# Kernel tuning notes

Measured on AMD Instinct MI355X. Metric: run time of the kernel, lower is better.

Reference implementation:

```python
import jax, jax.numpy as jnp
import numpy as np

HID = 128          # args.hidden_dim
B = 8              # batch_size
N = 256            # num_nodes per graph (uniform)
L = 48             # num_colours / levels per graph (uniform, logk=False)
CELLS = B * N * L  # 98304 'cell' nodes
E = 250000         # edges per edge type
STEPS = 2          # args.msg_passing_steps


def setup_inputs() -> dict:
    key = jax.random.key(0)
    ks = jax.random.split(key, 20)
    s = 0.05
    d = {}
    d["q"] = jax.random.randint(ks[0], (CELLS,), 0, 3)
    d["edge_src"] = jax.random.randint(ks[1], (2, E), 0, CELLS)
    d["edge_dst"] = jax.random.randint(ks[2], (2, E), 0, CELLS)
    d["embed"] = jax.random.normal(ks[3], (3, HID), jnp.float32) * s
    # per-edge-type 4-layer MLP (stacked along axis 0: [intra, inter])
    d["msg_W0"] = jax.random.normal(ks[4], (2, HID, 2 * HID), jnp.float32) * s
    d["msg_b0"] = jnp.zeros((2, HID), jnp.float32)
    d["msg_W1"] = jax.random.normal(ks[5], (2, HID, HID), jnp.float32) * s
    d["msg_b1"] = jnp.zeros((2, HID), jnp.float32)
    d["msg_W2"] = jax.random.normal(ks[6], (2, HID, HID), jnp.float32) * s
    d["msg_b2"] = jnp.zeros((2, HID), jnp.float32)
    d["msg_W3"] = jax.random.normal(ks[7], (2, HID, HID), jnp.float32) * s
    d["msg_b3"] = jnp.zeros((2, HID), jnp.float32)
    # LSTMCell, bias=False: input = cat(x, m_intra, m_inter) -> 3*HID
    d["lstm_Wih"] = jax.random.normal(ks[8], (4 * HID, 3 * HID), jnp.float32) * s
    d["lstm_Whh"] = jax.random.normal(ks[9], (4 * HID, HID), jnp.float32) * s
    d["score_w"] = jax.random.normal(ks[10], (1, HID), jnp.float32) * s
    return d


def reference(q, edge_src, edge_dst, embed, msg_W0, msg_b0, msg_W1, msg_b1,
              msg_W2, msg_b2, msg_W3, msg_b3, lstm_Wih, lstm_Whh, score_w):
    x = embed[q]  # [CELLS, HID]

    def edge_msgs(h):
        msgs = []
        for et in range(2):  # structural loop over the 2 edge types
            src, dst = edge_src[et], edge_dst[et]
            m = jnp.concatenate([h[src], h[dst]], axis=-1)  # [E, 2H]
            m = jax.nn.relu(m @ msg_W0[et].T + msg_b0[et])
            m = jax.nn.relu(m @ msg_W1[et].T + msg_b1[et])
            m = jax.nn.relu(m @ msg_W2[et].T + msg_b2[et])
            m = m @ msg_W3[et].T + msg_b3[et]
            msgs.append(jax.ops.segment_sum(m, dst, num_segments=CELLS))
        return msgs

    def step(carry, _):
        h, rh, rc = carry
        m_intra, m_inter = edge_msgs(h)
        lstm_in = jnp.concatenate([x, m_intra, m_inter], axis=-1)  # [CELLS, 3H]
        gates = lstm_in @ lstm_Wih.T + rh @ lstm_Whh.T              # [CELLS, 4H]
        i, f, g, o = jnp.split(gates, 4, axis=-1)
        nc = jax.nn.sigmoid(f) * rc + jax.nn.sigmoid(i) * jnp.tanh(g)
        nh = jax.nn.sigmoid(o) * jnp.tanh(nc)
        return (nh, nh, nc), nh

    zeros = jnp.zeros_like(x)
    _, outs = jax.lax.scan(step, (x, zeros, zeros), None, length=STEPS)
    # outs: [STEPS, CELLS, HID]; uniform sizes make get_padded_tensor a reshape:
    # [STEPS, B, L, N, HID] -> score -> view(STEPS, B*N*L)
    logits = (outs @ score_w[0]).reshape(STEPS, B * L * N)
    return logits
```

## Files before the change

kernel.cpp:

```cpp
#include <hip/hip_runtime.h>

#define HID 128
#define CELLS 98304
#define NE 250000
#define NSTEPS 2
#define NWIN 3912

typedef __attribute__((ext_vector_type(8))) short short8;
typedef __attribute__((ext_vector_type(4))) float f32x4;
typedef __attribute__((ext_vector_type(4))) unsigned int u32x4;
typedef unsigned short u16;

__device__ __forceinline__ int permf(int s) { return ((s & 7) << 4) | (s >> 3); }
__device__ __forceinline__ int nat_of_pos(int p) {
  int l = p & 63, hf = p >> 6;
  int slot = ((l >> 2) << 3) + (hf << 2) + (l & 3);
  return ((slot & 7) << 4) | (slot >> 3);
}

__device__ __forceinline__ u16 f2bf(float f) {
  unsigned int u = __builtin_bit_cast(unsigned int, f);
  u += 0x7fffu + ((u >> 16) & 1u);
  return (u16)(u >> 16);
}
__device__ __forceinline__ float bf2f(u16 s) {
  unsigned int u = ((unsigned int)s) << 16;
  return __builtin_bit_cast(float, u);
}
__device__ __forceinline__ unsigned int cvtpk_bf16(float lo, float hi) {
  unsigned int r;
  asm("v_cvt_pk_bf16_f32 %0, %1, %2" : "=v"(r) : "v"(lo), "v"(hi));
  return r;
}
__device__ __forceinline__ float sigm(float x) { return 1.f / (1.f + __expf(-x)); }
__device__ __forceinline__ float tanha(float x) { return 1.f - 2.f / (__expf(2.f * x) + 1.f); }

__device__ __forceinline__ void gload_lds16(const u16* g, u16* l) {
  __builtin_amdgcn_global_load_lds(
      (const __attribute__((address_space(1))) unsigned int*)(const void*)g,
      (__attribute__((address_space(3))) unsigned int*)(void*)l, 16, 0, 0);
}

__device__ __forceinline__ void stage_w(const u16* __restrict__ ws, u16* wl, int w, int lane) {
  #pragma unroll
  for (int i = 0; i < 2; ++i)
    gload_lds16(ws + i * 4096 + w * 512 + lane * 8, wl + i * 4096 + w * 512);
}

__global__ void prep_kernel(
    const float* __restrict__ W0, const float* __restrict__ W1,
    const float* __restrict__ W2, const float* __restrict__ W3,
    const float* __restrict__ b0, const float* __restrict__ b1,
    const float* __restrict__ b2, const float* __restrict__ b3,
    const float* __restrict__ Wih, const float* __restrict__ Whh,
    const float* __restrict__ embed, const float* __restrict__ sw,
    u16* __restrict__ W0b, u16* __restrict__ W123b,
    u16* __restrict__ Wcb, float* __restrict__ bp,
    u16* __restrict__ embp, float* __restrict__ swp)
{
  int idx = blockIdx.x * 256 + threadIdx.x;
  if (idx < 65536) {
    int et = idx >> 15, t = (idx >> 13) & 3, n = (idx >> 6) & 127, s = idx & 63;
    int g = s >> 3, j = s & 7;
    int gn = g ^ (n & 7);
    W0b[idx] = f2bf(W0[(et * 128 + n) * 256 + t * 64 + gn * 8 + j]);
    return;
  }
  idx -= 65536;
  if (idx < 98304) {
    int which = idx >> 15, r = idx & 32767;
    int et = r >> 14, hh = (r >> 13) & 1, n = (r >> 6) & 127, s = r & 63;
    int g = s >> 3, j = s & 7;
    int gn = g ^ (n & 7);
    const float* W = which == 0 ? W1 : (which == 1 ? W2 : W3);
    W123b[which * 32768 + r] = f2bf(W[(et * 128 + n) * 128 + permf(hh * 64 + gn * 8 + j)]);
    return;
  }
  idx -= 98304;
  if (idx < 262144) {
    int s = idx & 511, n = idx >> 9;
    int blk = s >> 7, s7 = s & 127;
    int k7 = (blk == 1 || blk == 2) ? nat_of_pos(s7) : s7;
    float v = (blk < 3) ? Wih[n * 384 + blk * 128 + k7] : Whh[n * 128 + k7];
    Wcb[idx] = f2bf(v);
    return;
  }
  idx -= 262144;
  if (idx < 1024) {
    int l = idx >> 8, r = idx & 255;
    int et = r >> 7, s = r & 127;
    const float* b = l == 0 ? b0 : (l == 1 ? b1 : (l == 2 ? b2 : b3));
    bp[idx] = b[et * 128 + permf(s)];
    return;
  }
  idx -= 1024;
  if (idx < 384) {
    embp[idx] = f2bf(embed[idx]);
    return;
  }
  idx -= 384;
  if (idx < 128) swp[idx] = sw[idx];
}

__global__ void init_kernel(const int* __restrict__ q, const u16* __restrict__ embp,
                            u16* __restrict__ xb, u16* __restrict__ h)
{
  int idx = blockIdx.x * 256 + threadIdx.x;
  int c = idx >> 7, s = idx & 127;
  u16 v = embp[q[c] * 128 + s];
  xb[idx] = v;
  h[idx] = v;
}

__global__ void hist_kernel(const int* __restrict__ edst, int* __restrict__ counts)
{
  int idx = blockIdx.x * 256 + threadIdx.x;
  if (idx >= 2 * NE) return;
  int et = (idx >= NE) ? 1 : 0;
  atomicAdd(&counts[et * CELLS + edst[idx]], 1);
}

__global__ void scan1_kernel(const int* __restrict__ counts, int* __restrict__ S,
                             int* __restrict__ btot)
{
  __shared__ int sh[1024];
  const int t = threadIdx.x, b = blockIdx.x;
  const int i = b * 1024 + t;
  int v = counts[i];
  sh[t] = v;
  __syncthreads();
  int acc = v;
  for (int off = 1; off < 1024; off <<= 1) {
    int add = (t >= off) ? sh[t - off] : 0;
    __syncthreads();
    acc += add;
    sh[t] = acc;
    __syncthreads();
  }
  S[i] = acc - v;
  if (t == 1023) btot[b] = acc;
}

__global__ void scan2_kernel(const int* __restrict__ btot, int* __restrict__ boffs,
                             int* __restrict__ S)
{
  __shared__ int sh[256];
  const int t = threadIdx.x;
  int v = (t < 192) ? btot[t] : 0;
  sh[t] = v;
  __syncthreads();
  int acc = v;
  for (int off = 1; off < 256; off <<= 1) {
    int add = (t >= off) ? sh[t - off] : 0;
    __syncthreads();
    acc += add;
    sh[t] = acc;
    __syncthreads();
  }
  if (t < 192) boffs[t] = acc - v;
  if (t == 0) S[2 * CELLS] = 2 * NE;
}

__global__ void scan3_kernel(int* __restrict__ S, const int* __restrict__ boffs)
{
  const int i = blockIdx.x * 1024 + threadIdx.x;
  S[i] += boffs[blockIdx.x];
}

__global__ void scatter_kernel(const int* __restrict__ esrc, const int* __restrict__ edst,
                               const int* __restrict__ S, int* __restrict__ fill,
                               int* __restrict__ ssrc, int* __restrict__ sdst)
{
  int idx = blockIdx.x * 256 + threadIdx.x;
  if (idx >= 2 * NE) return;
  int et = (idx >= NE) ? 1 : 0;
  int d = edst[idx];
  int pos = atomicAdd(&fill[et * CELLS + d], 1);
  int slot = S[et * CELLS + d] - et * NE + pos;
  sdst[et * NE + slot] = d;
  ssrc[et * NE + slot] = esrc[idx];
}

__device__ __forceinline__ void bias_relu_store(f32x4 (&acc)[4][8], const float* __restrict__ bl,
                                                u16* __restrict__ ab, int q, int c)
{
  float bias[8];
  #pragma unroll
  for (int j = 0; j < 8; ++j) bias[j] = bl[c * 8 + j];
  #pragma unroll
  for (int mt = 0; mt < 4; ++mt) {
    #pragma unroll
    for (int r = 0; r < 4; ++r) {
      const int rowl = mt * 16 + 4 * q + r;
      u32x4 t;
      #pragma unroll
      for (int p = 0; p < 4; ++p) {
        float v0 = acc[mt][2 * p][r] + bias[2 * p];
        float v1 = acc[mt][2 * p + 1][r] + bias[2 * p + 1];
        v0 = v0 > 0.f ? v0 : 0.f;
        v1 = v1 > 0.f ? v1 : 0.f;
        t[p] = cvtpk_bf16(v0, v1);
      }
      *(u32x4*)(ab + rowl * 128 + ((c ^ (rowl & 15)) << 3)) = t;
    }
  }
}

__launch_bounds__(512, 2)
__global__ void msg_kernel(
    const u16* __restrict__ h,
    const int* __restrict__ ssrc, const int* __restrict__ sdst,
    const int* __restrict__ S,
    const u16* __restrict__ W0b, const u16* __restrict__ W123b,
    const float* __restrict__ bp,
    u16* __restrict__ m0, u16* __restrict__ m1,
    int* __restrict__ side_dst, float* __restrict__ side_part)
{
  __shared__ u16 abuf[8][64 * 128];
  __shared__ u16 wbuf[2][128 * 64];
  const int et = blockIdx.y;
  const int tid = threadIdx.x;
  const int w = tid >> 6, lane = tid & 63, q = lane >> 4, c = lane & 15;
  const int ebase = blockIdx.x * 512 + w * 64;
  const int win = blockIdx.x * 8 + w;
  const int* __restrict__ src = ssrc + et * NE;
  const int* __restrict__ dst = sdst + et * NE;
  u16* __restrict__ msgs = (et == 0) ? m0 : m1;
  u16* ab = abuf[w];

  int eS = ebase + lane;
  if (eS >= NE) eS = NE - 1;
  const int srow = src[eS];

  int rowD[4];
  #pragma unroll
  for (int mt = 0; mt < 4; ++mt) {
    int e = ebase + mt * 16 + c;
    if (e >= NE) e = NE - 1;
    rowD[mt] = dst[e];
  }

  #pragma unroll
  for (int i = 0; i < 16; ++i) {
    const int r = i * 4 + (lane >> 4);
    const int grow = __shfl(srow, r);
    const int cg = lane & 15;
    gload_lds16(h + (size_t)grow * 128 + ((cg ^ (r & 15)) << 3), ab + i * 512);
  }
  stage_w(W0b + (et * 4 + 2) * 8192, wbuf[0], w, lane);

  const int eL = ebase + lane;
  const int dval = (eL < NE) ? dst[eL] : -1;
  int rpS = 0, rpE = 0;
  if (dval >= 0) {
    rpS = S[et * CELLS + dval] - et * NE;
    rpE = S[et * CELLS + dval + 1] - et * NE;
  }
  const int dlagged = __shfl_up(dval, 1);
  const bool headp = (lane == 0) | (dval != dlagged);
  const unsigned long long tails = (__ballot(headp) >> 1) | (1ull << 63);
  const unsigned long long intmask = __ballot(dval >= 0 && rpS >= ebase && rpE <= ebase + 64);

  const f32x4 zf = {0.f, 0.f, 0.f, 0.f};
  f32x4 acc[4][8];
  #pragma unroll
  for (int mt = 0; mt < 4; ++mt)
    #pragma unroll
    for (int nt = 0; nt < 8; ++nt) acc[mt][nt] = zf;

  asm volatile("s_waitcnt vmcnt(0)" ::: "memory");
  __syncthreads();

  #pragma unroll 1
  for (int i = 0; i < 10; ++i) {
    if (i < 9) {
      const int j = i + 1;
      const u16* wsrc;
      if (j < 4) {
        const int t = (j < 2) ? (j + 2) : (j - 2);
        wsrc = W0b + (et * 4 + t) * 8192;
      } else {
        const int li = j - 4;
        wsrc = W123b + (li >> 1) * 32768 + et * 16384 + (li & 1) * 8192;
      }
      stage_w(wsrc, wbuf[j & 1], w, lane);
    }
    if (i >= 4 && !(i & 1)) {
      bias_relu_store(acc, bp + ((i - 4) >> 1) * 256 + et * 128, ab, q, c);
      #pragma unroll
      for (int mt = 0; mt < 4; ++mt)
        #pragma unroll
        for (int nt = 0; nt < 8; ++nt) acc[mt][nt] = zf;
    }
    const u16* wb = wbuf[i & 1];
    #pragma unroll
    for (int ks = 0; ks < 2; ++ks) {
      short8 a[4], b[8];
      if (i < 2) {
        const int kqh = i * 64 + ks * 32 + q * 8;
        #pragma unroll
        for (int mt = 0; mt < 4; ++mt)
          a[mt] = *(const short8*)(h + (size_t)rowD[mt] * HID + kqh);
      } else {
        const int blk = (i & 1) * 8 + ks * 4 + q;
        #pragma unroll
        for (int mt = 0; mt < 4; ++mt) {
          const int row = mt * 16 + c;
          a[mt] = *(const short8*)(ab + row * 128 + ((blk ^ c) << 3));
        }
      }
      #pragma unroll
      for (int nt = 0; nt < 8; ++nt)
        b[nt] = *(const short8*)(wb + (nt * 16 + c) * 64 + (((ks * 4 + q) ^ (c & 7)) << 3));
      #pragma unroll
      for (int mt = 0; mt < 4; ++mt)
        #pragma unroll
        for (int nt = 0; nt < 8; ++nt)
          acc[mt][nt] = __builtin_amdgcn_mfma_f32_16x16x32_bf16(a[mt], b[nt], acc[mt][nt], 0, 0, 0);
    }
    asm volatile("s_waitcnt vmcnt(0)" ::: "memory");
    __syncthreads();
  }

  float bias[8];
  #pragma unroll
  for (int j = 0; j < 8; ++j) bias[j] = bp[3 * 256 + et * 128 + c * 8 + j];

  float* fab = (float*)ab;
  #pragma unroll
  for (int half = 0; half < 2; ++half) {
    #pragma unroll
    for (int mt = 0; mt < 4; ++mt) {
      #pragma unroll
      for (int r = 0; r < 4; ++r) {
        const int row = mt * 16 + 4 * q + r;
        f32x4 t;
        #pragma unroll
        for (int nti = 0; nti < 4; ++nti)
          t[nti] = acc[mt][half * 4 + nti][r] + bias[half * 4 + nti];
        *(f32x4*)(fab + row * 64 + c * 4) = t;
      }
    }
    float run = 0.f;
    int jstart = 0;
    #pragma unroll 1
    for (int jb = 0; jb < 64; jb += 8) {
      #pragma unroll
      for (int u = 0; u < 8; ++u) {
        const int j = jb + u;
        run += fab[j * 64 + lane];
        if ((tails >> j) & 1) {
          const int d = __builtin_amdgcn_readlane(dval, j);
          if (d >= 0) {
            if ((intmask >> j) & 1) {
              msgs[(size_t)d * HID + half * 64 + lane] = f2bf(run);
            } else {
              const int slot = (jstart == 0) ? 0 : 1;
              const size_t sb = ((size_t)et * NWIN + win) * 2 + slot;
              side_part[sb * 128 + half * 64 + lane] = run;
              if (lane == 0 && half == 0) side_dst[sb] = d;
            }
          }
          run = 0.f;
          jstart = j + 1;
        }
      }
    }
  }
}

__global__ void fixup_kernel(const int* __restrict__ S,
                             const int* __restrict__ side_dst,
                             const float* __restrict__ side_part,
                             u16* __restrict__ m0, u16* __restrict__ m1)
{
  const int b = blockIdx.x;
  const int et = b / NWIN, win = b - et * NWIN;
  const int t = threadIdx.x;
  u16* __restrict__ m = et ? m1 : m0;
  #pragma unroll
  for (int s = 0; s < 2; ++s) {
    const int d = side_dst[b * 2 + s];
    if (d < 0) continue;
    const int r0 = S[et * CELLS + d] - et * NE;
    if ((r0 >> 6) != win) continue;
    const int w1 = (S[et * CELLS + d + 1] - et * NE - 1) >> 6;
    float sum = 0.f;
    for (int wi = win; wi <= w1; ++wi) {
      const int base = (et * NWIN + wi) * 2;
      if (side_dst[base + 0] == d) sum += side_part[(size_t)(base + 0) * 128 + t];
      if (side_dst[base + 1] == d) sum += side_part[(size_t)(base + 1) * 128 + t];
    }
    m[(size_t)d * HID + t] = f2bf(sum);
  }
}

__launch_bounds__(512, 4)
__global__ void lstm_kernel(
    const int step,
    const u16* __restrict__ xb, const u16* __restrict__ mm0, const u16* __restrict__ mm1,
    u16* __restrict__ h, u16* __restrict__ rc,
    const u16* __restrict__ Wcb, const float* __restrict__ swp,
    float* __restrict__ out)
{
  __shared__ u16 at[64 * 512];
  const int tid = threadIdx.x;
  const int cb = blockIdx.x * 64;

  for (int base = tid * 8; base < 64 * 512; base += 4096) {
    const int cl = base >> 9, s = base & 511;
    const int cell = cb + cl;
    short8 t;
    if (s < 128) {
      t = *(const short8*)(xb + cell * 128 + s);
    } else if (s < 384) {
      const u16* mp = (s < 256 ? mm0 : mm1) + cell * 128 + (s & 127);
      t = *(const short8*)(mp);
    } else if (step == 0) {
      #pragma unroll
      for (int j = 0; j < 8; ++j) t[j] = 0;
    } else {
      t = *(const short8*)(h + cell * 128 + (s & 127));
    }
    const int blk = s >> 3;
    const int blks = (blk & 48) | ((blk ^ cl) & 15);
    *(short8*)(at + cl * 512 + blks * 8) = t;
  }
  __syncthreads();

  const int w = tid >> 6, lane = tid & 63, q = lane >> 4, c = lane & 15;
  const int wf = w;
  const f32x4 zf = {0.f, 0.f, 0.f, 0.f};
  f32x4 acc[4][4];
  #pragma unroll
  for (int mt = 0; mt < 4; ++mt)
    #pragma unroll
    for (int g = 0; g < 4; ++g) acc[mt][g] = zf;

  #pragma unroll
  for (int ks = 0; ks < 16; ++ks) {
    const int kq = ks * 32 + q * 8;
    const int blk = kq >> 3;
    short8 a[4], b[4];
    #pragma unroll
    for (int mt = 0; mt < 4; ++mt) {
      const int row = mt * 16 + c;
      const int blks = (blk & 48) | ((blk ^ c) & 15);
      a[mt] = *(const short8*)(at + row * 512 + blks * 8);
    }
    #pragma unroll
    for (int g = 0; g < 4; ++g)
      b[g] = *(const short8*)(Wcb + (g * 128 + wf * 16 + c) * 512 + kq);
    #pragma unroll
    for (int mt = 0; mt < 4; ++mt)
      #pragma unroll
      for (int g = 0; g < 4; ++g)
        acc[mt][g] = __builtin_amdgcn_mfma_f32_16x16x32_bf16(a[mt], b[g], acc[mt][g], 0, 0, 0);
  }
  __syncthreads();

  const float swc = swp[wf * 16 + c];
  const bool last = (step == NSTEPS - 1);
  float* pt = (float*)at;
  #pragma unroll
  for (int mt = 0; mt < 4; ++mt) {
    #pragma unroll
    for (int r = 0; r < 4; ++r) {
      const int cl = mt * 16 + 4 * q + r;
      const int cell = cb + cl;
      const float ig = sigm(acc[mt][0][r]);
      const float fg = sigm(acc[mt][1][r]);
      const float gg = tanha(acc[mt][2][r]);
      const float og = sigm(acc[mt][3][r]);
      u16* rcp = rc + (size_t)cell * HID + wf * 16 + c;
      const float c0 = (step == 0) ? 0.f : bf2f(rcp[0]);
      const float nc = fg * c0 + ig * gg;
      const float nhv = og * tanha(nc);
      if (!last) {
        rcp[0] = f2bf(nc);
        h[(size_t)cell * HID + wf * 16 + c] = f2bf(nhv);
      }
      float v = nhv * swc;
      v += __shfl_xor(v, 1); v += __shfl_xor(v, 2);
      v += __shfl_xor(v, 4); v += __shfl_xor(v, 8);
      if (c == 0) pt[wf * 64 + cl] = v;
    }
  }
  __syncthreads();
  if (tid < 64) {
    float s = 0.f;
    #pragma unroll
    for (int ww = 0; ww < 8; ++ww) s += pt[ww * 64 + tid];
    out[step * CELLS + cb + tid] = s;
  }
}

extern "C" void kernel_launch(void* const* d_in, const int* in_sizes, int n_in,
                              void* d_out, int out_size, void* d_ws, size_t ws_size,
                              hipStream_t stream)
{
  const int* q      = (const int*)d_in[0];
  const int* esrc   = (const int*)d_in[1];
  const int* edst   = (const int*)d_in[2];
  const float* embed= (const float*)d_in[3];
  const float* W0   = (const float*)d_in[4];
  const float* b0   = (const float*)d_in[5];
  const float* W1   = (const float*)d_in[6];
  const float* b1   = (const float*)d_in[7];
  const float* W2   = (const float*)d_in[8];
  const float* b2   = (const float*)d_in[9];
  const float* W3   = (const float*)d_in[10];
  const float* b3   = (const float*)d_in[11];
  const float* Wih  = (const float*)d_in[12];
  const float* Whh  = (const float*)d_in[13];
  const float* sw   = (const float*)d_in[14];

  char* ws = (char*)d_ws;
  size_t off = 0;
  auto alloc = [&](size_t bytes) {
    void* p = ws + off;
    off += (bytes + 255) & ~(size_t)255;
    return p;
  };
  u16*   h    = (u16*)  alloc((size_t)CELLS * HID * 2);
  u16*   xb   = (u16*)  alloc((size_t)CELLS * HID * 2);
  u16*   rc   = (u16*)  alloc((size_t)CELLS * HID * 2);
  u16*   m0   = (u16*)  alloc((size_t)CELLS * HID * 2);
  u16*   m1   = (u16*)  alloc((size_t)CELLS * HID * 2);
  u16*   W0b  = (u16*)  alloc(2 * 128 * 256 * 2);
  u16*   W123b= (u16*)  alloc((size_t)3 * 2 * 128 * 128 * 2);
  u16*   Wcb  = (u16*)  alloc(512 * 512 * 2);
  float* bp   = (float*)alloc(4 * 256 * 4);
  u16*   embp = (u16*)  alloc(384 * 2);
  float* swp  = (float*)alloc(128 * 4);
  int*   counts = (int*)alloc((size_t)2 * CELLS * 4);
  int*   Sarr   = (int*)alloc(((size_t)2 * CELLS + 1) * 4);
  int*   fill   = (int*)alloc((size_t)2 * CELLS * 4);
  int*   btot   = (int*)alloc(192 * 4);
  int*   boffs  = (int*)alloc(192 * 4);
  int*   ssrc   = (int*)alloc((size_t)2 * NE * 4);
  int*   sdst   = (int*)alloc((size_t)2 * NE * 4);
  int*   side_dst  = (int*)  alloc((size_t)2 * NWIN * 2 * 4);
  float* side_part = (float*)alloc((size_t)2 * NWIN * 2 * 128 * 4);

  prep_kernel<<<1670, 256, 0, stream>>>(W0, W1, W2, W3, b0, b1, b2, b3, Wih, Whh, embed, sw,
                                        W0b, W123b, Wcb, bp, embp, swp);
  init_kernel<<<(CELLS * HID) / 256, 256, 0, stream>>>(q, embp, xb, h);

  hipMemsetAsync(counts, 0, (size_t)2 * CELLS * 4, stream);
  hipMemsetAsync(fill, 0, (size_t)2 * CELLS * 4, stream);
  hist_kernel<<<(2 * NE + 255) / 256, 256, 0, stream>>>(edst, counts);
  scan1_kernel<<<192, 1024, 0, stream>>>(counts, Sarr, btot);
  scan2_kernel<<<1, 256, 0, stream>>>(btot, boffs, Sarr);
  scan3_kernel<<<192, 1024, 0, stream>>>(Sarr, boffs);
  scatter_kernel<<<(2 * NE + 255) / 256, 256, 0, stream>>>(esrc, edst, Sarr, fill, ssrc, sdst);

  hipMemsetAsync(m0, 0, (size_t)2 * CELLS * HID * 2, stream);
  hipMemsetAsync(side_dst, 0xFF, (size_t)2 * NWIN * 2 * 4, stream);

  for (int step = 0; step < NSTEPS; ++step) {
    msg_kernel<<<dim3((NE + 511) / 512, 2), 512, 0, stream>>>(h, ssrc, sdst, Sarr,
                                                              W0b, W123b, bp,
                                                              m0, m1, side_dst, side_part);
    fixup_kernel<<<2 * NWIN, 128, 0, stream>>>(Sarr, side_dst, side_part, m0, m1);
    lstm_kernel<<<CELLS / 64, 512, 0, stream>>>(step, xb, m0, m1, h, rc, Wcb, swp, (float*)d_out);
  }
}
```

Before: 701.7 us.

## Precompute per-node first-layer projections instead of per-edge W0 GEMM

The first MLP layer is linear in the concatenated [h_src, h_dst], so it splits into h_src·W0a + h_dst·W0b. A new proj_kernel computes these projections once per cell for both edge types, and msg_kernel then gathers the two projected rows, adds bias and applies ReLU. This removes the 256-wide first-layer GEMM from the per-edge work (250k edges per type versus 98k cells). In exchange it writes and reads a 4×CELLS×128 bf16 buffer each step, adds a kernel launch, and rounds the projection to bf16 before the sum.

```diff
diff --git a/kernel.cpp b/kernel.cpp
--- a/kernel.cpp
+++ b/kernel.cpp
@@ -54,16 +54,15 @@
     const float* __restrict__ b2, const float* __restrict__ b3,
     const float* __restrict__ Wih, const float* __restrict__ Whh,
     const float* __restrict__ embed, const float* __restrict__ sw,
-    u16* __restrict__ W0b, u16* __restrict__ W123b,
+    u16* __restrict__ Wpb, u16* __restrict__ W123b,
     u16* __restrict__ Wcb, float* __restrict__ bp,
     u16* __restrict__ embp, float* __restrict__ swp)
 {
   int idx = blockIdx.x * 256 + threadIdx.x;
   if (idx < 65536) {
-    int et = idx >> 15, t = (idx >> 13) & 3, n = (idx >> 6) & 127, s = idx & 63;
-    int g = s >> 3, j = s & 7;
-    int gn = g ^ (n & 7);
-    W0b[idx] = f2bf(W0[(et * 128 + n) * 256 + t * 64 + gn * 8 + j]);
+    int o = idx >> 7, k = idx & 127;
+    int et = o >> 8, kind = (o >> 7) & 1, slot = o & 127;
+    Wpb[idx] = f2bf(W0[(et * 128 + permf(slot)) * 256 + kind * 128 + k]);
     return;
   }
   idx -= 65536;
@@ -181,6 +180,61 @@
   ssrc[et * NE + slot] = esrc[idx];
 }
 
+__launch_bounds__(512, 4)
+__global__ void proj_kernel(const u16* __restrict__ h, const u16* __restrict__ Wpb,
+                            u16* __restrict__ pp)
+{
+  __shared__ u16 at[64 * 128];
+  const int tid = threadIdx.x;
+  const int cb = blockIdx.x * 64;
+  for (int base = tid * 8; base < 64 * 128; base += 4096) {
+    const int cl = base >> 7, s = base & 127;
+    short8 t = *(const short8*)(h + (size_t)(cb + cl) * 128 + s);
+    const int blk = s >> 3;
+    *(short8*)(at + cl * 128 + ((blk ^ (cl & 15)) << 3)) = t;
+  }
+  __syncthreads();
+
+  const int w = tid >> 6, lane = tid & 63, q = lane >> 4, c = lane & 15;
+  const f32x4 zf = {0.f, 0.f, 0.f, 0.f};
+  f32x4 acc[4][4];
+  #pragma unroll
+  for (int mt = 0; mt < 4; ++mt)
+    #pragma unroll
+    for (int no = 0; no < 4; ++no) acc[mt][no] = zf;
+
+  #pragma unroll
+  for (int ks = 0; ks < 4; ++ks) {
+    const int kq = ks * 32 + q * 8;
+    const int blk = kq >> 3;
+    short8 a[4], b[4];
+    #pragma unroll
+    for (int mt = 0; mt < 4; ++mt)
+      a[mt] = *(const short8*)(at + (mt * 16 + c) * 128 + ((blk ^ c) << 3));
+    #pragma unroll
+    for (int no = 0; no < 4; ++no)
+      b[no] = *(const short8*)(Wpb + (size_t)(w * 64 + no * 16 + c) * 128 + kq);
+    #pragma unroll
+    for (int mt = 0; mt < 4; ++mt)
+      #pragma unroll
+      for (int no = 0; no < 4; ++no)
+        acc[mt][no] = __builtin_amdgcn_mfma_f32_16x16x32_bf16(a[mt], b[no], acc[mt][no], 0, 0, 0);
+  }
+
+  const int g2 = w >> 1;
+  const int sbase = (w & 1) * 64;
+  #pragma unroll
+  for (int mt = 0; mt < 4; ++mt) {
+    #pragma unroll
+    for (int r = 0; r < 4; ++r) {
+      const int cell = cb + mt * 16 + 4 * q + r;
+      u16* op = pp + ((size_t)g2 * CELLS + cell) * 128 + sbase + c;
+      #pragma unroll
+      for (int no = 0; no < 4; ++no) op[no * 16] = f2bf(acc[mt][no][r]);
+    }
+  }
+}
+
 __device__ __forceinline__ void bias_relu_store(f32x4 (&acc)[4][8], const float* __restrict__ bl,
                                                 u16* __restrict__ ab, int q, int c)
 {
@@ -208,10 +262,10 @@
 
 __launch_bounds__(512, 2)
 __global__ void msg_kernel(
-    const u16* __restrict__ h,
+    const u16* __restrict__ pp,
     const int* __restrict__ ssrc, const int* __restrict__ sdst,
     const int* __restrict__ S,
-    const u16* __restrict__ W0b, const u16* __restrict__ W123b,
+    const u16* __restrict__ W123b,
     const float* __restrict__ bp,
     u16* __restrict__ m0, u16* __restrict__ m1,
     int* __restrict__ side_dst, float* __restrict__ side_part)
@@ -225,29 +279,16 @@
   const int win = blockIdx.x * 8 + w;
   const int* __restrict__ src = ssrc + et * NE;
   const int* __restrict__ dst = sdst + et * NE;
+  const u16* __restrict__ psb = pp + (size_t)(et * 2 + 0) * CELLS * 128;
+  const u16* __restrict__ pdb = pp + (size_t)(et * 2 + 1) * CELLS * 128;
   u16* __restrict__ msgs = (et == 0) ? m0 : m1;
   u16* ab = abuf[w];
+
+  stage_w(W123b + et * 16384, wbuf[0], w, lane);
 
   int eS = ebase + lane;
   if (eS >= NE) eS = NE - 1;
   const int srow = src[eS];
-
-  int rowD[4];
-  #pragma unroll
-  for (int mt = 0; mt < 4; ++mt) {
-    int e = ebase + mt * 16 + c;
-    if (e >= NE) e = NE - 1;
-    rowD[mt] = dst[e];
-  }
-
-  #pragma unroll
-  for (int i = 0; i < 16; ++i) {
-    const int r = i * 4 + (lane >> 4);
-    const int grow = __shfl(srow, r);
-    const int cg = lane & 15;
-    gload_lds16(h + (size_t)grow * 128 + ((cg ^ (r & 15)) << 3), ab + i * 512);
-  }
-  stage_w(W0b + (et * 4 + 2) * 8192, wbuf[0], w, lane);
 
   const int eL = ebase + lane;
   const int dval = (eL < NE) ? dst[eL] : -1;
@@ -261,6 +302,49 @@
   const unsigned long long tails = (__ballot(headp) >> 1) | (1ull << 63);
   const unsigned long long intmask = __ballot(dval >= 0 && rpS >= ebase && rpE <= ebase + 64);
 
+  #pragma unroll
+  for (int i = 0; i < 16; ++i) {
+    const int r = i * 4 + (lane >> 4);
+    const int grow = __shfl(srow, r);
+    const int cg = lane & 15;
+    gload_lds16(psb + (size_t)grow * 128 + ((cg ^ (r & 15)) << 3), ab + i * 512);
+  }
+
+  short8 pdr[16];
+  #pragma unroll
+  for (int i = 0; i < 16; ++i) {
+    const int r = i * 4 + (lane >> 4);
+    int drow = __shfl(dval, r);
+    drow = drow < 0 ? 0 : drow;
+    pdr[i] = *(const short8*)(pdb + (size_t)drow * 128 + ((lane & 15) << 3));
+  }
+
+  asm volatile("s_waitcnt vmcnt(0)" ::: "memory");
+  __syncthreads();
+
+  {
+    const int cg = lane & 15;
+    float bz[8];
+    #pragma unroll
+    for (int j = 0; j < 8; ++j) bz[j] = bp[et * 128 + cg * 8 + j];
+    #pragma unroll
+    for (int i = 0; i < 16; ++i) {
+      const int r = i * 4 + (lane >> 4);
+      u16* p = ab + r * 128 + ((cg ^ (r & 15)) << 3);
+      short8 sv = *(const short8*)p;
+      u32x4 o;
+      #pragma unroll
+      for (int x = 0; x < 4; ++x) {
+        float v0 = bf2f((u16)sv[2 * x])     + bf2f((u16)pdr[i][2 * x])     + bz[2 * x];
+        float v1 = bf2f((u16)sv[2 * x + 1]) + bf2f((u16)pdr[i][2 * x + 1]) + bz[2 * x + 1];
+        v0 = v0 > 0.f ? v0 : 0.f;
+        v1 = v1 > 0.f ? v1 : 0.f;
+        o[x] = cvtpk_bf16(v0, v1);
+      }
+      *(u32x4*)p = o;
+    }
+  }
+
   const f32x4 zf = {0.f, 0.f, 0.f, 0.f};
   f32x4 acc[4][8];
   #pragma unroll
@@ -268,25 +352,14 @@
     #pragma unroll
     for (int nt = 0; nt < 8; ++nt) acc[mt][nt] = zf;
 
-  asm volatile("s_waitcnt vmcnt(0)" ::: "memory");
-  __syncthreads();
-
   #pragma unroll 1
-  for (int i = 0; i < 10; ++i) {
-    if (i < 9) {
+  for (int i = 0; i < 6; ++i) {
+    if (i < 5) {
       const int j = i + 1;
-      const u16* wsrc;
-      if (j < 4) {
-        const int t = (j < 2) ? (j + 2) : (j - 2);
-        wsrc = W0b + (et * 4 + t) * 8192;
-      } else {
-        const int li = j - 4;
-        wsrc = W123b + (li >> 1) * 32768 + et * 16384 + (li & 1) * 8192;
-      }
-      stage_w(wsrc, wbuf[j & 1], w, lane);
-    }
-    if (i >= 4 && !(i & 1)) {
-      bias_relu_store(acc, bp + ((i - 4) >> 1) * 256 + et * 128, ab, q, c);
+      stage_w(W123b + (j >> 1) * 32768 + et * 16384 + (j & 1) * 8192, wbuf[j & 1], w, lane);
+    }
+    if (i == 2 || i == 4) {
+      bias_relu_store(acc, bp + (i >> 1) * 256 + et * 128, ab, q, c);
       #pragma unroll
       for (int mt = 0; mt < 4; ++mt)
         #pragma unroll
@@ -295,19 +368,12 @@
     const u16* wb = wbuf[i & 1];
     #pragma unroll
     for (int ks = 0; ks < 2; ++ks) {
+      const int blk = (i & 1) * 8 + ks * 4 + q;
       short8 a[4], b[8];
-      if (i < 2) {
-        const int kqh = i * 64 + ks * 32 + q * 8;
-        #pragma unroll
-        for (int mt = 0; mt < 4; ++mt)
-          a[mt] = *(const short8*)(h + (size_t)rowD[mt] * HID + kqh);
-      } else {
-        const int blk = (i & 1) * 8 + ks * 4 + q;
-        #pragma unroll
-        for (int mt = 0; mt < 4; ++mt) {
-          const int row = mt * 16 + c;
-          a[mt] = *(const short8*)(ab + row * 128 + ((blk ^ c) << 3));
-        }
+      #pragma unroll
+      for (int mt = 0; mt < 4; ++mt) {
+        const int row = mt * 16 + c;
+        a[mt] = *(const short8*)(ab + row * 128 + ((blk ^ c) << 3));
       }
       #pragma unroll
       for (int nt = 0; nt < 8; ++nt)
@@ -527,7 +593,8 @@
   u16*   rc   = (u16*)  alloc((size_t)CELLS * HID * 2);
   u16*   m0   = (u16*)  alloc((size_t)CELLS * HID * 2);
   u16*   m1   = (u16*)  alloc((size_t)CELLS * HID * 2);
-  u16*   W0b  = (u16*)  alloc(2 * 128 * 256 * 2);
+  u16*   pp   = (u16*)  alloc((size_t)4 * CELLS * 128 * 2);
+  u16*   Wpb  = (u16*)  alloc(512 * 128 * 2);
   u16*   W123b= (u16*)  alloc((size_t)3 * 2 * 128 * 128 * 2);
   u16*   Wcb  = (u16*)  alloc(512 * 512 * 2);
   float* bp   = (float*)alloc(4 * 256 * 4);
@@ -544,7 +611,7 @@
   float* side_part = (float*)alloc((size_t)2 * NWIN * 2 * 128 * 4);
 
   prep_kernel<<<1670, 256, 0, stream>>>(W0, W1, W2, W3, b0, b1, b2, b3, Wih, Whh, embed, sw,
-                                        W0b, W123b, Wcb, bp, embp, swp);
+                                        Wpb, W123b, Wcb, bp, embp, swp);
   init_kernel<<<(CELLS * HID) / 256, 256, 0, stream>>>(q, embp, xb, h);
 
   hipMemsetAsync(counts, 0, (size_t)2 * CELLS * 4, stream);
@@ -559,8 +626,9 @@
   hipMemsetAsync(side_dst, 0xFF, (size_t)2 * NWIN * 2 * 4, stream);
 
   for (int step = 0; step < NSTEPS; ++step) {
-    msg_kernel<<<dim3((NE + 511) / 512, 2), 512, 0, stream>>>(h, ssrc, sdst, Sarr,
-                                                              W0b, W123b, bp,
+    proj_kernel<<<CELLS / 64, 512, 0, stream>>>(h, Wpb, pp);
+    msg_kernel<<<dim3((NE + 511) / 512, 2), 512, 0, stream>>>(pp, ssrc, sdst, Sarr,
+                                                              W123b, bp,
                                                               m0, m1, side_dst, side_part);
     fixup_kernel<<<2 * NWIN, 128, 0, stream>>>(Sarr, side_dst, side_part, m0, m1);
     lstm_kernel<<<CELLS / 64, 512, 0, stream>>>(step, xb, m0, m1, h, rc, Wcb, swp, (float*)d_out);
```

Result: slower. 768.8 us (+9.6%).

## Double-buffer LSTM GEMM with async global-to-LDS staging of weights and activations

Applied to the files above, without the earlier changes.

Restructures the LSTM gate GEMM into eight K-chunks of 64. Both the activation tile and a pre-swizzled chunk of the combined weight matrix are staged into LDS with direct global-to-LDS loads, double-buffered so the next chunk loads while MFMAs run on the current one. Before, weights were read straight from global memory into registers. The weight prep layout changes to a chunked, XOR-swizzled order, and a zero row stands in for h at step 0. The cost is about 144KB of LDS per block, with launch bounds lowered to 2 blocks per SM, plus one barrier per chunk.

```diff
diff --git a/kernel.cpp b/kernel.cpp
--- a/kernel.cpp
+++ b/kernel.cpp
@@ -78,8 +78,11 @@
   }
   idx -= 98304;
   if (idx < 262144) {
-    int s = idx & 511, n = idx >> 9;
-    int blk = s >> 7, s7 = s & 127;
+    int kc = idx >> 15, r = idx & 32767;
+    int n = r >> 6, s = r & 63;
+    int gp = s >> 3, j = s & 7;
+    int k = kc * 64 + ((gp ^ (n & 7)) << 3) + j;
+    int blk = k >> 7, s7 = k & 127;
     int k7 = (blk == 1 || blk == 2) ? nat_of_pos(s7) : s7;
     float v = (blk < 3) ? Wih[n * 384 + blk * 128 + k7] : Whh[n * 128 + k7];
     Wcb[idx] = f2bf(v);
@@ -395,41 +398,21 @@
   }
 }
 
-__launch_bounds__(512, 4)
+__launch_bounds__(512, 2)
 __global__ void lstm_kernel(
     const int step,
     const u16* __restrict__ xb, const u16* __restrict__ mm0, const u16* __restrict__ mm1,
     u16* __restrict__ h, u16* __restrict__ rc,
     const u16* __restrict__ Wcb, const float* __restrict__ swp,
+    const u16* __restrict__ zrow,
     float* __restrict__ out)
 {
-  __shared__ u16 at[64 * 512];
+  __shared__ u16 wbuf[2][512 * 64];
+  __shared__ u16 abuf[2][64 * 64];
   const int tid = threadIdx.x;
   const int cb = blockIdx.x * 64;
-
-  for (int base = tid * 8; base < 64 * 512; base += 4096) {
-    const int cl = base >> 9, s = base & 511;
-    const int cell = cb + cl;
-    short8 t;
-    if (s < 128) {
-      t = *(const short8*)(xb + cell * 128 + s);
-    } else if (s < 384) {
-      const u16* mp = (s < 256 ? mm0 : mm1) + cell * 128 + (s & 127);
-      t = *(const short8*)(mp);
-    } else if (step == 0) {
-      #pragma unroll
-      for (int j = 0; j < 8; ++j) t[j] = 0;
-    } else {
-      t = *(const short8*)(h + cell * 128 + (s & 127));
-    }
-    const int blk = s >> 3;
-    const int blks = (blk & 48) | ((blk ^ cl) & 15);
-    *(short8*)(at + cl * 512 + blks * 8) = t;
-  }
-  __syncthreads();
-
   const int w = tid >> 6, lane = tid & 63, q = lane >> 4, c = lane & 15;
-  const int wf = w;
+
   const f32x4 zf = {0.f, 0.f, 0.f, 0.f};
   f32x4 acc[4][4];
   #pragma unroll
@@ -437,31 +420,69 @@
     #pragma unroll
     for (int g = 0; g < 4; ++g) acc[mt][g] = zf;
 
-  #pragma unroll
-  for (int ks = 0; ks < 16; ++ks) {
-    const int kq = ks * 32 + q * 8;
-    const int blk = kq >> 3;
-    short8 a[4], b[4];
-    #pragma unroll
-    for (int mt = 0; mt < 4; ++mt) {
-      const int row = mt * 16 + c;
-      const int blks = (blk & 48) | ((blk ^ c) & 15);
-      a[mt] = *(const short8*)(at + row * 512 + blks * 8);
-    }
-    #pragma unroll
-    for (int g = 0; g < 4; ++g)
-      b[g] = *(const short8*)(Wcb + (g * 128 + wf * 16 + c) * 512 + kq);
-    #pragma unroll
-    for (int mt = 0; mt < 4; ++mt)
-      #pragma unroll
-      for (int g = 0; g < 4; ++g)
-        acc[mt][g] = __builtin_amdgcn_mfma_f32_16x16x32_bf16(a[mt], b[g], acc[mt][g], 0, 0, 0);
-  }
+  const int scl = tid >> 3, slg = tid & 7;
+  const int scol0 = ((slg ^ (scl & 7)) << 3);
+  #define STAGE_A(kc, buf)                                                         \
+    {                                                                              \
+      const int col = (((kc) & 1) << 6) + scol0;                                   \
+      const int sel = (kc) >> 1;                                                   \
+      const u16* srcp;                                                             \
+      if (sel == 0)      srcp = xb  + (size_t)(cb + scl) * 128 + col;              \
+      else if (sel == 1) srcp = mm0 + (size_t)(cb + scl) * 128 + col;              \
+      else if (sel == 2) srcp = mm1 + (size_t)(cb + scl) * 128 + col;              \
+      else srcp = (step == 0) ? (zrow + col) : (h + (size_t)(cb + scl) * 128 + col); \
+      gload_lds16(srcp, abuf[buf] + w * 512);                                      \
+    }
+  #define STAGE_W(kc, buf)                                                         \
+    {                                                                              \
+      _Pragma("unroll")                                                            \
+      for (int i = 0; i < 8; ++i)                                                  \
+        gload_lds16(Wcb + (size_t)(kc) * 32768 + i * 4096 + tid * 8,               \
+                    wbuf[buf] + i * 4096 + w * 512);                               \
+    }
+
+  STAGE_A(0, 0);
+  STAGE_W(0, 0);
+  asm volatile("s_waitcnt vmcnt(0)" ::: "memory");
   __syncthreads();
 
-  const float swc = swp[wf * 16 + c];
+  #pragma unroll 1
+  for (int kc = 0; kc < 8; ++kc) {
+    if (kc < 7) {
+      STAGE_A(kc + 1, (kc + 1) & 1);
+      STAGE_W(kc + 1, (kc + 1) & 1);
+    }
+    const u16* ac = abuf[kc & 1];
+    const u16* wc = wbuf[kc & 1];
+    #pragma unroll
+    for (int kk = 0; kk < 2; ++kk) {
+      const int lg = kk * 4 + q;
+      short8 a[4], b[4];
+      #pragma unroll
+      for (int mt = 0; mt < 4; ++mt) {
+        const int row = mt * 16 + c;
+        a[mt] = *(const short8*)(ac + row * 64 + ((lg ^ (row & 7)) << 3));
+      }
+      #pragma unroll
+      for (int g = 0; g < 4; ++g) {
+        const int n = g * 128 + w * 16 + c;
+        b[g] = *(const short8*)(wc + n * 64 + ((lg ^ (n & 7)) << 3));
+      }
+      #pragma unroll
+      for (int mt = 0; mt < 4; ++mt)
+        #pragma unroll
+        for (int g = 0; g < 4; ++g)
+          acc[mt][g] = __builtin_amdgcn_mfma_f32_16x16x32_bf16(a[mt], b[g], acc[mt][g], 0, 0, 0);
+    }
+    asm volatile("s_waitcnt vmcnt(0)" ::: "memory");
+    __syncthreads();
+  }
+  #undef STAGE_A
+  #undef STAGE_W
+
+  const float swc = swp[w * 16 + c];
   const bool last = (step == NSTEPS - 1);
-  float* pt = (float*)at;
+  float* pt = (float*)abuf;
   #pragma unroll
   for (int mt = 0; mt < 4; ++mt) {
     #pragma unroll
@@ -472,18 +493,18 @@
       const float fg = sigm(acc[mt][1][r]);
       const float gg = tanha(acc[mt][2][r]);
       const float og = sigm(acc[mt][3][r]);
-      u16* rcp = rc + (size_t)cell * HID + wf * 16 + c;
+      u16* rcp = rc + (size_t)cell * HID + w * 16 + c;
       const float c0 = (step == 0) ? 0.f : bf2f(rcp[0]);
       const float nc = fg * c0 + ig * gg;
       const float nhv = og * tanha(nc);
       if (!last) {
         rcp[0] = f2bf(nc);
-        h[(size_t)cell * HID + wf * 16 + c] = f2bf(nhv);
+        h[(size_t)cell * HID + w * 16 + c] = f2bf(nhv);
       }
       float v = nhv * swc;
       v += __shfl_xor(v, 1); v += __shfl_xor(v, 2);
       v += __shfl_xor(v, 4); v += __shfl_xor(v, 8);
-      if (c == 0) pt[wf * 64 + cl] = v;
+      if (c == 0) pt[w * 64 + cl] = v;
     }
   }
   __syncthreads();
@@ -533,6 +554,7 @@
   float* bp   = (float*)alloc(4 * 256 * 4);
   u16*   embp = (u16*)  alloc(384 * 2);
   float* swp  = (float*)alloc(128 * 4);
+  u16*   zrow = (u16*)  alloc(128 * 2);
   int*   counts = (int*)alloc((size_t)2 * CELLS * 4);
   int*   Sarr   = (int*)alloc(((size_t)2 * CELLS + 1) * 4);
   int*   fill   = (int*)alloc((size_t)2 * CELLS * 4);
@@ -557,12 +579,14 @@
 
   hipMemsetAsync(m0, 0, (size_t)2 * CELLS * HID * 2, stream);
   hipMemsetAsync(side_dst, 0xFF, (size_t)2 * NWIN * 2 * 4, stream);
+  hipMemsetAsync(zrow, 0, 128 * 2, stream);
 
   for (int step = 0; step < NSTEPS; ++step) {
     msg_kernel<<<dim3((NE + 511) / 512, 2), 512, 0, stream>>>(h, ssrc, sdst, Sarr,
                                                               W0b, W123b, bp,
                                                               m0, m1, side_dst, side_part);
     fixup_kernel<<<2 * NWIN, 128, 0, stream>>>(Sarr, side_dst, side_part, m0, m1);
-    lstm_kernel<<<CELLS / 64, 512, 0, stream>>>(step, xb, m0, m1, h, rc, Wcb, swp, (float*)d_out);
-  }
-}
+    lstm_kernel<<<CELLS / 64, 512, 0, stream>>>(step, xb, m0, m1, h, rc, Wcb, swp, zrow,
+                                                (float*)d_out);
+  }
+}
```

Result: no change. 702.2 us (+0.1%).
